# Kernel optimization log

Hardware: AMD Instinct MI355X
Metric: run time of the kernel (lower is better)

Reference implementation:

```python
import jax, jax.numpy as jnp
import numpy as np

B, NI, NO = 4, 256, 256          # batch, num_in, num_out
DIN, DQ, DH, DOUT = 256, 256, 256, 256


def setup_inputs() -> dict:
    key = jax.random.key(0)
    ks = jax.random.split(key, 6)
    def w(k, shape, fan_in):
        return jax.random.normal(k, shape, jnp.float32) / np.sqrt(fan_in).astype(np.float32)
    return {
        "x": jax.random.normal(ks[0], (B, NI, DIN), jnp.float32),
        "query": jax.random.normal(ks[1], (B, NO, DQ), jnp.float32),
        # pre_cond_mlp: Linear(DIN -> DH)
        "W_pre": w(ks[2], (DIN, DH), DIN), "b_pre": jnp.zeros((DH,), jnp.float32),
        # cond_embed: Linear(DQ -> DH)
        "W_emb": w(ks[3], (DQ, DH), DQ), "b_emb": jnp.zeros((DH,), jnp.float32),
        # post_cond_mlp: Linear(2*DH -> DH) + GELU + Linear(DH -> DOUT)
        "W1": w(ks[4], (2 * DH, DH), 2 * DH), "b1": jnp.zeros((DH,), jnp.float32),
        "W2": w(ks[5], (DH, DOUT), DH), "b2": jnp.zeros((DOUT,), jnp.float32),
    }


def reference(x, query, W_pre, b_pre, W_emb, b_emb, W1, b1, W2, b2):
    # pre_cond_mlp(x): [B, NI, DH]
    xp = x @ W_pre + b_pre
    # cond_embed(query): [B, NO, DH]
    c = query @ W_emb + b_emb
    # Original torch code: repeat xp over NO, c over NI, concat -> [B,NI,NO,2*DH],
    # then Linear(2*DH->DH). Algebraically identical (and far cheaper) to split W1
    # and broadcast-add the two projections:
    W1x, W1c = W1[:DH], W1[DH:]          # [DH, DH] each
    h = (xp @ W1x)[:, :, None, :] + (c @ W1c)[:, None, :, :] + b1  # [B, NI, NO, DH]
    h = jax.nn.gelu(h, approximate=False)  # torch nn.GELU default = exact erf
    return h @ W2 + b2                     # [B, NI, NO, DOUT]
```

## Files before the change

kernel.cpp:

```cpp
#include <hip/hip_runtime.h>
#include <hip/hip_bf16.h>
#include <cstdint>
#include <cstddef>


typedef __bf16  bf16x8 __attribute__((ext_vector_type(8)));
typedef float   f32x16 __attribute__((ext_vector_type(16)));

__device__ __forceinline__ float fast_gelu(float x) {
    const float x2 = x * x;
    const float m  = __builtin_fmaf(x2, -0.1029433f, -2.3022072f);
    const float e  = __builtin_amdgcn_exp2f(x * m);
    return x * __builtin_amdgcn_rcpf(1.0f + e);
}

__global__ __launch_bounds__(256) void prep_kernel(
    const float* __restrict__ x, const float* __restrict__ query,
    const float* __restrict__ W_pre, const float* __restrict__ b_pre,
    const float* __restrict__ W_emb, const float* __restrict__ b_emb,
    const float* __restrict__ W1, const float* __restrict__ b1,
    const float* __restrict__ W2,
    float* __restrict__ u, float* __restrict__ v,
    unsigned short* __restrict__ w2t)
{
    const int b = blockIdx.x;
    const int t = threadIdx.x;

    if (b >= 512) {
        const int n0 = (b - 512) * 4;
        const float4 wv = *reinterpret_cast<const float4*>(W2 + (size_t)t * 256 + n0);
        const float vals[4] = {wv.x, wv.y, wv.z, wv.w};
#pragma unroll
        for (int j = 0; j < 4; ++j) {
            const __bf16 bv = (__bf16)vals[j];
            w2t[(size_t)(n0 + j) * 256 + t] = __builtin_bit_cast(unsigned short, bv);
        }
        return;
    }

    const bool isq = (b >= 256);
    const float* __restrict__ A   = isq ? query : x;
    const float* __restrict__ Wa  = isq ? W_emb : W_pre;
    const float* __restrict__ ba  = isq ? b_emb : b_pre;
    const float* __restrict__ W1p = isq ? (W1 + 256 * 256) : W1;
    float* __restrict__ outp      = isq ? v : u;
    const int r0 = (isq ? (b - 256) : b) * 4;

    __shared__ float as[4][256];
    __shared__ float xs[4][256];

#pragma unroll
    for (int r = 0; r < 4; ++r)
        as[r][t] = A[(size_t)(r0 + r) * 256 + t];
    __syncthreads();

    float acc[4] = {0.f, 0.f, 0.f, 0.f};
    {
        float wcur[8];
#pragma unroll
        for (int q = 0; q < 8; ++q) wcur[q] = Wa[(size_t)q * 256 + t];
        for (int k0 = 0; k0 < 248; k0 += 8) {
            float wnxt[8];
#pragma unroll
            for (int q = 0; q < 8; ++q)
                wnxt[q] = Wa[(size_t)(k0 + 8 + q) * 256 + t];
#pragma unroll
            for (int q = 0; q < 8; ++q)
#pragma unroll
                for (int r = 0; r < 4; ++r)
                    acc[r] = __builtin_fmaf(as[r][k0 + q], wcur[q], acc[r]);
#pragma unroll
            for (int q = 0; q < 8; ++q) wcur[q] = wnxt[q];
        }
#pragma unroll
        for (int q = 0; q < 8; ++q)
#pragma unroll
            for (int r = 0; r < 4; ++r)
                acc[r] = __builtin_fmaf(as[r][248 + q], wcur[q], acc[r]);
    }
    const float bav = ba[t];
#pragma unroll
    for (int r = 0; r < 4; ++r) xs[r][t] = acc[r] + bav;
    __syncthreads();

    float acc2[4] = {0.f, 0.f, 0.f, 0.f};
    {
        float wcur[8];
#pragma unroll
        for (int q = 0; q < 8; ++q) wcur[q] = W1p[(size_t)q * 256 + t];
        for (int k0 = 0; k0 < 248; k0 += 8) {
            float wnxt[8];
#pragma unroll
            for (int q = 0; q < 8; ++q)
                wnxt[q] = W1p[(size_t)(k0 + 8 + q) * 256 + t];
#pragma unroll
            for (int q = 0; q < 8; ++q)
#pragma unroll
                for (int r = 0; r < 4; ++r)
                    acc2[r] = __builtin_fmaf(xs[r][k0 + q], wcur[q], acc2[r]);
#pragma unroll
            for (int q = 0; q < 8; ++q) wcur[q] = wnxt[q];
        }
#pragma unroll
        for (int q = 0; q < 8; ++q)
#pragma unroll
            for (int r = 0; r < 4; ++r)
                acc2[r] = __builtin_fmaf(xs[r][248 + q], wcur[q], acc2[r]);
    }
    const float b1v = isq ? 0.f : b1[t];
#pragma unroll
    for (int r = 0; r < 4; ++r)
        outp[(size_t)(r0 + r) * 256 + t] = acc2[r] + b1v;
}

__global__ __launch_bounds__(256, 2) void fused_kernel(
    const float* __restrict__ U, const float* __restrict__ V,
    const unsigned short* __restrict__ W2T, const float* __restrict__ b2,
    float* __restrict__ out)
{
    __shared__ uint4 wlds[4096];
    __shared__ uint4 hlds[1024];
    unsigned int* const h32 = reinterpret_cast<unsigned int*>(hlds);

    const int t    = threadIdx.x;
    const int lane = t & 63;
    const int w    = t >> 6;
    const int l31  = lane & 31;
    const int hi   = lane >> 5;
    const int d    = l31;

    const int bid = blockIdx.x;
    const int ch  = bid & 1;
    const int grp = bid >> 1;
    const int n0  = ch * 128;

#pragma unroll
    for (int it = 0; it < 16; ++it) {
        const int idx = it * 256 + t;
        const int n   = idx >> 5;
        const int gp  = idx & 31;
        const int g   = (gp & 24) | ((gp ^ n) & 7);
        __builtin_amdgcn_global_load_lds(
            (const __attribute__((address_space(1))) unsigned int*)
                (W2T + (size_t)(n0 + n) * 256 + g * 8),
            (__attribute__((address_space(3))) unsigned int*)(wlds + idx),
            16, 0, 0);
    }

    float bvv[4];
#pragma unroll
    for (int cg = 0; cg < 4; ++cg) bvv[cg] = b2[n0 + cg * 32 + l31];

    float2 vvA[16], vvB[16];
    float2 u2A, u2B;
    const float* urow;
    const float* vrow;

    auto task_ptrs = [&](int task) {
        const int P    = grp * 8 + task;
        const int tile = P >> 1;
        const int jh   = P & 1;
        const int bb   = tile >> 8;
        urow = U + (size_t)tile * 256;
        vrow = V + ((size_t)(bb * 256 + jh * 128)) * 256;
    };

    auto load_t = [&](int kk, float2& u2, float2 (&vv)[16]) {
        u2 = *reinterpret_cast<const float2*>(urow + kk + 2 * d);
#pragma unroll
        for (int p = 0; p < 16; ++p) {
            const int row = w * 32 + p * 2 + hi;
            vv[p] = *reinterpret_cast<const float2*>(
                vrow + (size_t)row * 256 + kk + 2 * d);
        }
    };

    auto gelu_write = [&](const float2& u2, const float2 (&vv)[16]) {
#pragma unroll
        for (int p = 0; p < 16; ++p) {
            const int row = w * 32 + p * 2 + hi;
            union { unsigned int u32; __bf16 h[2]; } pk;
            pk.h[0] = (__bf16)fast_gelu(u2.x + vv[p].x);
            pk.h[1] = (__bf16)fast_gelu(u2.y + vv[p].y);
            h32[row * 32 + (((d >> 2) ^ (row & 7)) << 2) + (d & 3)] = pk.u32;
        }
    };

    f32x16 acc[4];

    auto mfma_chunk = [&](int kk) {
        const int kg0 = kk >> 3;
#pragma unroll
        for (int s = 0; s < 4; ++s) {
            const int gl   = 2 * s + hi;
            const int arow = w * 32 + l31;
            const bf16x8 afrag = __builtin_bit_cast(
                bf16x8, hlds[arow * 8 + (gl ^ (arow & 7))]);
            const int gk = kg0 + gl;
#pragma unroll
            for (int cg = 0; cg < 4; ++cg) {
                const int nloc = cg * 32 + l31;
                const int slot = (gk & 24) | ((gk ^ nloc) & 7);
                const bf16x8 bfrag = __builtin_bit_cast(
                    bf16x8, wlds[nloc * 32 + slot]);
                acc[cg] = __builtin_amdgcn_mfma_f32_32x32x16_bf16(
                    afrag, bfrag, acc[cg], 0, 0, 0);
            }
        }
    };

    task_ptrs(0);
    load_t(0, u2A, vvA);

    __syncthreads();

    for (int task = 0; task < 8; ++task) {
#pragma unroll
        for (int i = 0; i < 4; ++i) acc[i] = (f32x16)0.f;

        load_t(64, u2B, vvB);
        gelu_write(u2A, vvA);
        mfma_chunk(0);
        load_t(128, u2A, vvA);
        gelu_write(u2B, vvB);
        mfma_chunk(64);
        load_t(192, u2B, vvB);
        gelu_write(u2A, vvA);
        mfma_chunk(128);
        const int P    = grp * 8 + task;
        const int tile = P >> 1;
        const int jh   = P & 1;
        if (task < 7) {
            task_ptrs(task + 1);
            load_t(0, u2A, vvA);
        }
        gelu_write(u2B, vvB);
        mfma_chunk(192);

        const size_t obase = ((size_t)tile << 16) + (size_t)(jh * 128) * 256;
#pragma unroll
        for (int cg = 0; cg < 4; ++cg) {
            const int col = n0 + cg * 32 + l31;
#pragma unroll
            for (int rr = 0; rr < 16; ++rr) {
                const int row = w * 32 + 4 * hi + (rr & 3) + 8 * (rr >> 2);
                __builtin_nontemporal_store(acc[cg][rr] + bvv[cg],
                    out + obase + (size_t)row * 256 + col);
            }
        }
    }
}

extern "C" void kernel_launch(void* const* d_in, const int* in_sizes, int n_in,
                              void* d_out, int out_size, void* d_ws, size_t ws_size,
                              hipStream_t stream)
{
    const float* x     = (const float*)d_in[0];
    const float* query = (const float*)d_in[1];
    const float* W_pre = (const float*)d_in[2];
    const float* b_pre = (const float*)d_in[3];
    const float* W_emb = (const float*)d_in[4];
    const float* b_emb = (const float*)d_in[5];
    const float* W1    = (const float*)d_in[6];
    const float* b1    = (const float*)d_in[7];
    const float* W2    = (const float*)d_in[8];
    const float* b2    = (const float*)d_in[9];
    float* out = (float*)d_out;

    char* ws = (char*)d_ws;
    float* u            = (float*)(ws);
    float* v            = (float*)(ws + (1 << 20));
    unsigned short* w2t = (unsigned short*)(ws + 2 * (1 << 20));

    prep_kernel<<<576, 256, 0, stream>>>(x, query, W_pre, b_pre, W_emb, b_emb,
                                         W1, b1, W2, u, v, w2t);
    fused_kernel<<<512, 256, 0, stream>>>(u, v, w2t, b2, out);
}
```

Before: 112.1 us.

## Replace persistent fused kernel with one-tile-per-block 512-thread launch

The fused GELU+GEMM kernel no longer loops over 8 tasks per persistent block. It launches 4096 blocks of 512 threads, each computing a single 128x128 output tile with waves split 4x2 over rows and columns. The H tile in LDS is now shared across waves, so block barriers are added around each gelu-write/MFMA phase. This is meant to raise parallelism and occupancy, at the cost of reloading the W2 slice into LDS per block, losing cross-task prefetch overlap, and adding synchronization.

Measured after the change: 113.4 us. About the same (+1.2%).

```diff
diff --git a/kernel.cpp b/kernel.cpp
--- a/kernel.cpp
+++ b/kernel.cpp
@@ -113,7 +113,7 @@
         outp[(size_t)(r0 + r) * 256 + t] = acc2[r] + b1v;
 }
 
-__global__ __launch_bounds__(256, 2) void fused_kernel(
+__global__ __launch_bounds__(512, 4) void fused_kernel(
     const float* __restrict__ U, const float* __restrict__ V,
     const unsigned short* __restrict__ W2T, const float* __restrict__ b2,
     float* __restrict__ out)
@@ -127,16 +127,20 @@
     const int w    = t >> 6;
     const int l31  = lane & 31;
     const int hi   = lane >> 5;
-    const int d    = l31;
-
-    const int bid = blockIdx.x;
-    const int ch  = bid & 1;
-    const int grp = bid >> 1;
-    const int n0  = ch * 128;
-
-#pragma unroll
-    for (int it = 0; it < 16; ++it) {
-        const int idx = it * 256 + t;
+    const int wr   = w >> 1;
+    const int wc   = w & 1;
+
+    const int bid  = blockIdx.x;
+    const int tile = bid >> 2;
+    const int jh   = (bid >> 1) & 1;
+    const int ch   = bid & 1;
+    const int bb   = tile >> 8;
+    const int n0   = ch * 128;
+    const int j0   = jh * 128;
+
+#pragma unroll
+    for (int it = 0; it < 8; ++it) {
+        const int idx = it * 512 + t;
         const int n   = idx >> 5;
         const int gp  = idx & 31;
         const int g   = (gp & 24) | ((gp ^ n) & 7);
@@ -147,38 +151,33 @@
             16, 0, 0);
     }
 
-    float bvv[4];
-#pragma unroll
-    for (int cg = 0; cg < 4; ++cg) bvv[cg] = b2[n0 + cg * 32 + l31];
-
-    float2 vvA[16], vvB[16];
+    const float* __restrict__ urow  = U + (size_t)tile * 256;
+    const float* __restrict__ vbase = V + ((size_t)(bb * 256 + j0)) * 256;
+
+    const int d  = t & 31;
+    const int rb = t >> 5;
+
+    float bv[2];
+#pragma unroll
+    for (int cg = 0; cg < 2; ++cg) bv[cg] = b2[n0 + wc * 64 + cg * 32 + l31];
+
+    float2 vvA[8], vvB[8];
     float2 u2A, u2B;
-    const float* urow;
-    const float* vrow;
-
-    auto task_ptrs = [&](int task) {
-        const int P    = grp * 8 + task;
-        const int tile = P >> 1;
-        const int jh   = P & 1;
-        const int bb   = tile >> 8;
-        urow = U + (size_t)tile * 256;
-        vrow = V + ((size_t)(bb * 256 + jh * 128)) * 256;
+
+    auto load_chunk = [&](int kk, float2& u2, float2 (&vv)[8]) {
+        u2 = *reinterpret_cast<const float2*>(urow + kk + 2 * d);
+#pragma unroll
+        for (int p = 0; p < 8; ++p) {
+            const int row = rb + p * 16;
+            vv[p] = *reinterpret_cast<const float2*>(
+                vbase + (size_t)row * 256 + kk + 2 * d);
+        }
     };
 
-    auto load_t = [&](int kk, float2& u2, float2 (&vv)[16]) {
-        u2 = *reinterpret_cast<const float2*>(urow + kk + 2 * d);
-#pragma unroll
-        for (int p = 0; p < 16; ++p) {
-            const int row = w * 32 + p * 2 + hi;
-            vv[p] = *reinterpret_cast<const float2*>(
-                vrow + (size_t)row * 256 + kk + 2 * d);
-        }
-    };
-
-    auto gelu_write = [&](const float2& u2, const float2 (&vv)[16]) {
-#pragma unroll
-        for (int p = 0; p < 16; ++p) {
-            const int row = w * 32 + p * 2 + hi;
+    auto gelu_write = [&](const float2& u2, const float2 (&vv)[8]) {
+#pragma unroll
+        for (int p = 0; p < 8; ++p) {
+            const int row = rb + p * 16;
             union { unsigned int u32; __bf16 h[2]; } pk;
             pk.h[0] = (__bf16)fast_gelu(u2.x + vv[p].x);
             pk.h[1] = (__bf16)fast_gelu(u2.y + vv[p].y);
@@ -186,20 +185,22 @@
         }
     };
 
-    f32x16 acc[4];
+    f32x16 acc[2];
+#pragma unroll
+    for (int i = 0; i < 2; ++i) acc[i] = (f32x16)0.f;
 
     auto mfma_chunk = [&](int kk) {
         const int kg0 = kk >> 3;
 #pragma unroll
         for (int s = 0; s < 4; ++s) {
             const int gl   = 2 * s + hi;
-            const int arow = w * 32 + l31;
+            const int arow = wr * 32 + l31;
             const bf16x8 afrag = __builtin_bit_cast(
                 bf16x8, hlds[arow * 8 + (gl ^ (arow & 7))]);
             const int gk = kg0 + gl;
 #pragma unroll
-            for (int cg = 0; cg < 4; ++cg) {
-                const int nloc = cg * 32 + l31;
+            for (int cg = 0; cg < 2; ++cg) {
+                const int nloc = wc * 64 + cg * 32 + l31;
                 const int slot = (gk & 24) | ((gk ^ nloc) & 7);
                 const bf16x8 bfrag = __builtin_bit_cast(
                     bf16x8, wlds[nloc * 32 + slot]);
@@ -209,44 +210,37 @@
         }
     };
 
-    task_ptrs(0);
-    load_t(0, u2A, vvA);
-
-    __syncthreads();
-
-    for (int task = 0; task < 8; ++task) {
-#pragma unroll
-        for (int i = 0; i < 4; ++i) acc[i] = (f32x16)0.f;
-
-        load_t(64, u2B, vvB);
-        gelu_write(u2A, vvA);
-        mfma_chunk(0);
-        load_t(128, u2A, vvA);
-        gelu_write(u2B, vvB);
-        mfma_chunk(64);
-        load_t(192, u2B, vvB);
-        gelu_write(u2A, vvA);
-        mfma_chunk(128);
-        const int P    = grp * 8 + task;
-        const int tile = P >> 1;
-        const int jh   = P & 1;
-        if (task < 7) {
-            task_ptrs(task + 1);
-            load_t(0, u2A, vvA);
-        }
-        gelu_write(u2B, vvB);
-        mfma_chunk(192);
-
-        const size_t obase = ((size_t)tile << 16) + (size_t)(jh * 128) * 256;
-#pragma unroll
-        for (int cg = 0; cg < 4; ++cg) {
-            const int col = n0 + cg * 32 + l31;
-#pragma unroll
-            for (int rr = 0; rr < 16; ++rr) {
-                const int row = w * 32 + 4 * hi + (rr & 3) + 8 * (rr >> 2);
-                __builtin_nontemporal_store(acc[cg][rr] + bvv[cg],
-                    out + obase + (size_t)row * 256 + col);
-            }
+    load_chunk(0, u2A, vvA);
+    __syncthreads();
+
+    load_chunk(64, u2B, vvB);
+    gelu_write(u2A, vvA);
+    __syncthreads();
+    mfma_chunk(0);
+    __syncthreads();
+    load_chunk(128, u2A, vvA);
+    gelu_write(u2B, vvB);
+    __syncthreads();
+    mfma_chunk(64);
+    __syncthreads();
+    load_chunk(192, u2B, vvB);
+    gelu_write(u2A, vvA);
+    __syncthreads();
+    mfma_chunk(128);
+    __syncthreads();
+    gelu_write(u2B, vvB);
+    __syncthreads();
+    mfma_chunk(192);
+
+    const size_t obase = ((size_t)tile << 16) + (size_t)j0 * 256;
+#pragma unroll
+    for (int cg = 0; cg < 2; ++cg) {
+        const int col = n0 + wc * 64 + cg * 32 + l31;
+#pragma unroll
+        for (int rr = 0; rr < 16; ++rr) {
+            const int row = wr * 32 + 4 * hi + (rr & 3) + 8 * (rr >> 2);
+            __builtin_nontemporal_store(acc[cg][rr] + bv[cg],
+                                        out + obase + (size_t)row * 256 + col);
         }
     }
 }
@@ -274,5 +268,5 @@
 
     prep_kernel<<<576, 256, 0, stream>>>(x, query, W_pre, b_pre, W_emb, b_emb,
                                          W1, b1, W2, u, v, w2t);
-    fused_kernel<<<512, 256, 0, stream>>>(u, v, w2t, b2, out);
-}
+    fused_kernel<<<4096, 512, 0, stream>>>(u, v, w2t, b2, out);
+}
```
